# Performance work log

Measured on AMD Instinct MI355X. Metric: run time of the kernel, lower is better.

Reference implementation:

```python
import jax, jax.numpy as jnp
import numpy as np

A = 9
C = 80
TOPK = 1000            # topk_candidates
NMS_THRESH = 0.5
SCORE_THRESH = 0.05
DET_PER_IMG = 100      # detections_per_img
BBOX_XFORM_CLIP = float(np.log(1000.0 / 16.0))
CLASS_OFFSET = 4096.0  # > any clipped coordinate -> class-aware NMS trick


def setup_inputs() -> dict:
    key = jax.random.key(0)
    ks = jax.random.split(key, 4)
    B = 8
    levels = [(128, 128, 4096, 8), (64, 64, 2048, 16), (32, 32, 1024, 32)]  # H, W, K, stride
    inp = {}
    for i, (H, W, K, stride) in enumerate(levels):
        k1, k2, k3, k4, k5, k6, k7, k8 = jax.random.split(ks[i], 8)
        # plausible anchor boxes (x1, y1, x2, y2) with positive width/height
        cx = jax.random.uniform(k1, (B, H, W, A)) * (W * stride)
        cy = jax.random.uniform(k2, (B, H, W, A)) * (H * stride)
        w = 16.0 + jax.random.uniform(k3, (B, H, W, A)) * 112.0
        h = 16.0 + jax.random.uniform(k4, (B, H, W, A)) * 112.0
        anch = jnp.stack([cx - 0.5 * w, cy - 0.5 * h, cx + 0.5 * w, cy + 0.5 * h], axis=-1)
        # [B, H, W, A, 4] -> [B, 4A, H, W] (A groups of 4 along channel, matching permute(1,2,0) + reshape(-1,4))
        inp[f"anchors_{i}"] = jnp.transpose(anch.reshape(B, H, W, 4 * A), (0, 3, 1, 2)).astype(jnp.float32)
        coords = jnp.stack(
            [jax.random.randint(k5, (B, K), 0, H), jax.random.randint(k6, (B, K), 0, W)], axis=-1
        ).astype(jnp.int32)
        inp[f"coords_{i}"] = coords
        inp[f"score_logits_{i}"] = (jax.random.normal(k7, (B, K, A * C)) * 2.0 - 2.0).astype(jnp.float32)
        inp[f"regs_{i}"] = (jax.random.normal(k8, (B, K, A * 4)) * 0.2).astype(jnp.float32)
    inp["image_shapes"] = jnp.full((B, 2), 1024.0, dtype=jnp.float32)  # (h, w) per image
    return inp


def _decode(boxes, deltas, img_hw):
    # boxes, deltas: [N, 4] (x1, y1, x2, y2) / (dx, dy, dw, dh)
    x1, y1, x2, y2 = boxes[:, 0], boxes[:, 1], boxes[:, 2], boxes[:, 3]
    w = x2 - x1
    h = y2 - y1
    cx = x1 + 0.5 * w
    cy = y1 + 0.5 * h
    dx, dy = deltas[:, 0], deltas[:, 1]
    dw = jnp.minimum(deltas[:, 2], BBOX_XFORM_CLIP)
    dh = jnp.minimum(deltas[:, 3], BBOX_XFORM_CLIP)
    pcx = dx * w + cx
    pcy = dy * h + cy
    pw = jnp.exp(dw) * w
    ph = jnp.exp(dh) * h
    ih, iw = img_hw[0], img_hw[1]
    nx1 = jnp.clip(pcx - 0.5 * pw, 0.0, iw)
    ny1 = jnp.clip(pcy - 0.5 * ph, 0.0, ih)
    nx2 = jnp.clip(pcx + 0.5 * pw, 0.0, iw)
    ny2 = jnp.clip(pcy + 0.5 * ph, 0.0, ih)
    return jnp.stack([nx1, ny1, nx2, ny2], axis=-1)


def _level(anchor_map, coords, logits, regs, img_hw):
    # anchor_map: [4A, H, W]; coords: [K, 2]; logits: [K, A*C]; regs: [K, A*4]
    bb = jnp.transpose(anchor_map, (1, 2, 0))[coords[:, 0], coords[:, 1]]  # [K, 4A]
    boxes = bb.reshape(-1, 4)            # [K*A, 4]
    deltas = regs.reshape(-1, 4)         # [K*A, 4]
    dec = _decode(boxes, deltas, img_hw)
    scores = jax.nn.sigmoid(logits.reshape(-1, C))  # [K*A, C]
    flat = scores.reshape(-1)                       # [K*A*C]
    k = min(TOPK, flat.shape[0])
    top_s, idx = jax.lax.top_k(flat, k)
    return dec[idx // C], top_s, (idx % C)


def _pairwise_iou(b):
    area = (b[:, 2] - b[:, 0]) * (b[:, 3] - b[:, 1])
    lt = jnp.maximum(b[:, None, :2], b[None, :, :2])
    rb = jnp.minimum(b[:, None, 2:], b[None, :, 2:])
    wh = jnp.clip(rb - lt, 0.0)
    inter = wh[..., 0] * wh[..., 1]
    return inter / (area[:, None] + area[None, :] - inter + 1e-9)


def _nms(boxes, scores, labels):
    # class-aware NMS with fixed-size output [DET_PER_IMG, 6]
    order = jnp.argsort(-scores)
    b = boxes[order]
    s = scores[order]
    l = labels[order]
    iou = _pairwise_iou(b + l.astype(b.dtype)[:, None] * CLASS_OFFSET)  # [N, N]
    N = s.shape[0]
    idxs = jnp.arange(N)
    valid = s > SCORE_THRESH

    def body(i, keep):
        sup = (iou[i] > NMS_THRESH) & (idxs > i) & keep[i]
        return keep & ~sup

    keep = jax.lax.fori_loop(0, N, body, valid)
    masked = jnp.where(keep, s, -1.0)
    top_s, top_i = jax.lax.top_k(masked, DET_PER_IMG)
    pad = top_s > 0.0
    out_b = jnp.where(pad[:, None], b[top_i], 0.0)
    out_l = jnp.where(pad, l[top_i], -1).astype(b.dtype)
    return jnp.concatenate([out_b, top_s[:, None], out_l[:, None]], axis=-1)  # [DET, 6]


def _per_image(a0, a1, a2, c0, c1, c2, s0, s1, s2, r0, r1, r2, hw):
    parts = [
        _level(a, c, sl, r, hw)
        for a, c, sl, r in zip((a0, a1, a2), (c0, c1, c2), (s0, s1, s2), (r0, r1, r2))
    ]
    boxes = jnp.concatenate([p[0] for p in parts], axis=0)
    scores = jnp.concatenate([p[1] for p in parts], axis=0)
    labels = jnp.concatenate([p[2] for p in parts], axis=0)
    return _nms(boxes, scores, labels)


def reference(anchors_0, anchors_1, anchors_2, coords_0, coords_1, coords_2,
              score_logits_0, score_logits_1, score_logits_2,
              regs_0, regs_1, regs_2, image_shapes):
    # returns [B, DET_PER_IMG, 6] = (x1, y1, x2, y2, score, label); padded rows have score -1, label -1
    return jax.vmap(_per_image)(
        anchors_0, anchors_1, anchors_2,
        coords_0, coords_1, coords_2,
        score_logits_0, score_logits_1, score_logits_2,
        regs_0, regs_1, regs_2, image_shapes,
    )
```

## Files before the change

kernel.cpp:

```cpp
#include <hip/hip_runtime.h>

typedef unsigned long long u64;
typedef unsigned int u32;

#define NIMG 8
#define NLVL 3
#define TOPKN 1000
#define NC3 3000
#define DETS 100
#define PRETH 3.0f
#define NBINS 3072
#define LCAP 2048
#define MROWS 256
#define MLDS 128
#define NW 47
#define NWP 48
#define NSUB 32
#define SUBCAP 1536
#define GPAD 16

#define NBLK0 5760
#define NBLK1 2880
#define NBLK2 1440
#define NBLKTOT 10080

__device__ __forceinline__ u32 fmap(float f) {
  u32 b = __float_as_uint(f);
  return (b & 0x80000000u) ? ~b : (b | 0x80000000u);
}
__device__ __forceinline__ float funmap(u32 u) {
  u32 b = (u & 0x80000000u) ? (u & 0x7FFFFFFFu) : ~u;
  return __uint_as_float(b);
}

__global__ __launch_bounds__(256) void k_prefilter(
    const float* __restrict__ lg0, const float* __restrict__ lg1,
    const float* __restrict__ lg2, u64* __restrict__ dense,
    u32* __restrict__ gcnt) {
  const int tid = threadIdx.x, wave = tid >> 6, lane = tid & 63;
  int blk = blockIdx.x;
  const float* lg; int imgElems, lblk, lvl;
  if (blk < NBLK0)              { lg = lg0; imgElems = 2949120; lblk = blk; lvl = 0; }
  else if (blk < NBLK0 + NBLK1) { lg = lg1; imgElems = 1474560; lblk = blk - NBLK0; lvl = 1; }
  else                          { lg = lg2; imgElems = 737280;  lblk = blk - NBLK0 - NBLK1; lvl = 2; }
  int ce = lblk * 4096 + wave * 1024;
  int img = ce / imgElems;
  int flatBase = ce - img * imgElems;
  const float* src = lg + (size_t)img * imgElems;
  const int dst = img * NLVL + lvl;
  const int sub = (lblk * 4 + wave) & (NSUB - 1);
  u64 lmask = (1ull << lane) - 1ull;
  float va[16];
#pragma unroll
  for (int r = 0; r < 4; ++r) {
    const float4 v = *(const float4*)(src + flatBase + r * 256 + lane * 4);
    va[r * 4 + 0] = v.x; va[r * 4 + 1] = v.y;
    va[r * 4 + 2] = v.z; va[r * 4 + 3] = v.w;
  }
  u64 bm[16];
  int total = 0;
#pragma unroll
  for (int u = 0; u < 16; ++u) {
    bm[u] = __ballot(va[u] > PRETH);
    total += __popcll(bm[u]);
  }
  u32 base = 0;
  if (lane == 0 && total)
    base = atomicAdd(&gcnt[(dst * NSUB + sub) * GPAD], (u32)total);
  base = (u32)__shfl((int)base, 0);
  u64* db = dense + ((size_t)dst * NSUB + sub) * SUBCAP;
  int off = 0;
#pragma unroll
  for (int u = 0; u < 16; ++u) {
    u64 m = bm[u];
    if ((m >> lane) & 1ull) {
      int idx = flatBase + (u >> 2) * 256 + lane * 4 + (u & 3);
      u32 pos = base + (u32)(off + __popcll(m & lmask));
      if (pos < SUBCAP) db[pos] = ((u64)fmap(va[u]) << 32) | (u64)(~(u32)idx);
    }
    off += __popcll(m);
  }
}

__global__ __launch_bounds__(1024) void k_select(
    const u64* __restrict__ dense, const u32* __restrict__ gcnt,
    u64* __restrict__ topk) {
  __shared__ u32 hist[NBINS];
  __shared__ u64 lk[LCAP];
  __shared__ u32 wsum[16], wpre[16];
  __shared__ u32 scnt[NSUB];
  __shared__ int sT, sM;
  const int bi = blockIdx.x;
  const int tid = threadIdx.x, wave = tid >> 6, lane = tid & 63;

  const u64 SAFE = ((u64)0x3E5FFFFFu << 32) | 0xFFFFFFFFull;
  if (tid < TOPKN) topk[(size_t)bi * TOPKN + tid] = SAFE;
  for (int i = tid; i < NBINS; i += 1024) hist[i] = 0;
  if (tid < NSUB) {
    u32 c = gcnt[(bi * NSUB + tid) * GPAD];
    scnt[tid] = c > SUBCAP ? SUBCAP : c;
  }
  if (tid == 0) { sM = 0; sT = 0; }
  __syncthreads();

  const u64* src = dense + (size_t)bi * NSUB * SUBCAP;
  for (int s = wave; s < NSUB; s += 16) {
    u32 c = scnt[s];
    const u64* sp = src + (size_t)s * SUBCAP;
    for (u32 i = lane; i < c; i += 64) {
      u32 bin = ((u32)(sp[i] >> 32) - 0xC0000000u) >> 13;
      if (bin > NBINS - 1) bin = NBINS - 1;
      atomicAdd(&hist[bin], 1u);
    }
  }
  __syncthreads();

  const int h0 = NBINS - 1 - tid * 3;
  u32 a0 = hist[h0], a1 = hist[h0 - 1], a2 = hist[h0 - 2];
  u32 s = a0 + a1 + a2;
  u32 inc = s;
#pragma unroll
  for (int d = 1; d < 64; d <<= 1) {
    u32 t = (u32)__shfl_up((int)inc, d);
    if (lane >= d) inc += t;
  }
  if (lane == 63) wsum[wave] = inc;
  __syncthreads();
  if (tid < 16) {
    u32 w = wsum[tid];
    u32 wi = w;
#pragma unroll
    for (int d = 1; d < 16; d <<= 1) {
      u32 t = (u32)__shfl_up((int)wi, d);
      if (tid >= d) wi += t;
    }
    wpre[tid] = wi - w;
  }
  __syncthreads();
  u32 excl = wpre[wave] + (inc - s);
  if (excl < TOPKN && excl + s >= TOPKN) {
    u32 acc = excl + a0;
    int T;
    if (acc >= TOPKN) T = h0;
    else { acc += a1; T = (acc >= TOPKN) ? h0 - 1 : h0 - 2; }
    sT = T;
  }
  __syncthreads();
  const int T = sT;

  for (int s2 = wave; s2 < NSUB; s2 += 16) {
    u32 c = scnt[s2];
    const u64* sp = src + (size_t)s2 * SUBCAP;
    for (u32 i = lane; i < c; i += 64) {
      u64 key = sp[i];
      u32 bin = ((u32)(key >> 32) - 0xC0000000u) >> 13;
      if (bin > NBINS - 1) bin = NBINS - 1;
      if ((int)bin >= T) {
        int q = atomicAdd(&sM, 1);
        if (q < LCAP) lk[q] = key;
      }
    }
  }
  __syncthreads();
  int M = sM; if (M > LCAP) M = LCAP;
  u64 k0 = 0, k1 = 0;
  const bool have0 = tid < M, have1 = tid + 1024 < M;
  if (have0) k0 = lk[tid];
  if (have1) k1 = lk[tid + 1024];
  int r0 = 0, r1 = 0;
  for (int j = 0; j < M; ++j) {
    u64 kj = lk[j];
    r0 += (kj > k0);
    r1 += (kj > k1);
  }
  if (have0 && r0 < TOPKN) topk[(size_t)bi * TOPKN + r0] = k0;
  if (have1 && r1 < TOPKN) topk[(size_t)bi * TOPKN + r1] = k1;
}

__global__ __launch_bounds__(1024) void k_build(
    const u64* __restrict__ topk,
    const float* __restrict__ an0, const float* __restrict__ an1, const float* __restrict__ an2,
    const int* __restrict__ co0, const int* __restrict__ co1, const int* __restrict__ co2,
    const float* __restrict__ rg0, const float* __restrict__ rg1, const float* __restrict__ rg2,
    const float* __restrict__ ishape,
    float4* __restrict__ sbox, float* __restrict__ sscore, int* __restrict__ slabel) {
  __shared__ u64 keys[NC3];
  const int b = blockIdx.x, tid = threadIdx.x;
  const double ih = (double)ishape[b * 2 + 0];
  const double iw = (double)ishape[b * 2 + 1];
  const double CLIPV = 4.1351665567423563;
  float4 mb[3]; float ms[3]; int ml[3]; u64 mk[3]; bool mv[3];
  for (int q = 0; q < 3; ++q) {
    int c = tid + q * 1024;
    mv[q] = (c < NC3);
    mk[q] = 0ull;
    if (!mv[q]) continue;
    int l = c / 1000, pos = c - l * 1000;
    u64 key = topk[(size_t)(b * NLVL + l) * TOPKN + pos];
    u32 hi = (u32)(key >> 32);
    u32 flat = ~((u32)key);
    float logit = funmap(hi);
    int cls = (int)(flat % 80u);
    int bidx = (int)(flat / 80u);
    int k = bidx / 9, a = bidx - k * 9;
    const float* an; const int* co; const float* rg; int K, H, W;
    if (l == 0)      { an = an0; co = co0; rg = rg0; K = 4096; H = 128; W = 128; }
    else if (l == 1) { an = an1; co = co1; rg = rg1; K = 2048; H = 64;  W = 64;  }
    else             { an = an2; co = co2; rg = rg2; K = 1024; H = 32;  W = 32;  }
    if (k >= K) k = K - 1;
    int y = co[(b * K + k) * 2 + 0], x = co[(b * K + k) * 2 + 1];
    int HW = H * W;
    const float* ap = an + (size_t)(b * 36 + a * 4) * HW + y * W + x;
    double x1 = (double)ap[0], y1 = (double)ap[HW];
    double x2 = (double)ap[2 * HW], y2 = (double)ap[3 * HW];
    const float* rp = rg + (size_t)(b * K + k) * 36 + a * 4;
    double dx = (double)rp[0], dy = (double)rp[1];
    double dw = fmin((double)rp[2], CLIPV), dh = fmin((double)rp[3], CLIPV);
    double w = x2 - x1, h = y2 - y1;
    double cx = x1 + 0.5 * w, cy = y1 + 0.5 * h;
    double pcx = dx * w + cx, pcy = dy * h + cy;
    double pw = exp(dw) * w, ph = exp(dh) * h;
    double nx1 = fmin(fmax(pcx - 0.5 * pw, 0.0), iw);
    double ny1 = fmin(fmax(pcy - 0.5 * ph, 0.0), ih);
    double nx2 = fmin(fmax(pcx + 0.5 * pw, 0.0), iw);
    double ny2 = fmin(fmax(pcy + 0.5 * ph, 0.0), ih);
    mb[q] = make_float4((float)nx1, (float)ny1, (float)nx2, (float)ny2);
    ms[q] = (float)(1.0 / (1.0 + exp(-(double)logit)));
    ml[q] = cls;
    mk[q] = ((u64)hi << 32) | (u64)(~(u32)c);
    keys[c] = mk[q];
  }
  __syncthreads();
  for (int q = 0; q < 3; ++q) {
    if (!mv[q]) continue;
    int c = tid + q * 1024;
    int l = c / 1000, pos = c - l * 1000;
    int rank = pos;
    u64 key = mk[q];
#pragma unroll
    for (int m = 0; m < 3; ++m) {
      if (m == l) continue;
      int lo = 0, hi2 = 1000, base = m * 1000;
      while (lo < hi2) {
        int mid = (lo + hi2) >> 1;
        if (keys[base + mid] > key) lo = mid + 1; else hi2 = mid;
      }
      rank += lo;
    }
    sbox[(size_t)b * NC3 + rank] = mb[q];
    sscore[(size_t)b * NC3 + rank] = ms[q];
    slabel[(size_t)b * NC3 + rank] = ml[q];
  }
}

__global__ __launch_bounds__(256) void k_mask(
    const float4* __restrict__ sbox, const int* __restrict__ slabel,
    u64* __restrict__ mask) {
  __shared__ float4 qb[NC3];
  __shared__ float ar[NC3];
  const int img = blockIdx.x >> 4;
  const int r0 = (blockIdx.x & 15) * 16;
  const int tid = threadIdx.x, wave = tid >> 6, lane = tid & 63;
  for (int i = tid; i < NC3; i += 256) {
    float4 bx = sbox[(size_t)img * NC3 + i];
    float off = (float)slabel[(size_t)img * NC3 + i] * 4096.0f;
    float4 q = make_float4(bx.x + off, bx.y + off, bx.z + off, bx.w + off);
    qb[i] = q;
    ar[i] = (q.z - q.x) * (q.w - q.y);
  }
  __syncthreads();
  u64* mbase = mask + (size_t)img * MROWS * NWP;
  for (int q = 0; q < 4; ++q) {
    int i = r0 + wave * 4 + q;
    float4 bi = qb[i];
    float ai = ar[i];
    for (int w = 0; w < NW; ++w) {
      int j = w * 64 + lane;
      bool pred = false;
      if (j > i && j < NC3) {
        float4 bj = qb[j];
        float ltx = fmaxf(bi.x, bj.x), lty = fmaxf(bi.y, bj.y);
        float rbx = fminf(bi.z, bj.z), rby = fminf(bi.w, bj.w);
        float wx = fmaxf(rbx - ltx, 0.f), wy = fmaxf(rby - lty, 0.f);
        float inter = wx * wy;
        float denom = ((ai + ar[j]) - inter) + 1e-9f;
        pred = (inter / denom) > 0.5f;
      }
      u64 m = __ballot(pred);
      if (lane == 0) mbase[(size_t)i * NWP + w] = m;
    }
  }
}

__global__ __launch_bounds__(256) void k_serial(
    const float4* __restrict__ sbox, const float* __restrict__ sscore,
    const int* __restrict__ slabel, const u64* __restrict__ mask,
    float* __restrict__ out) {
  __shared__ u64 sm_mask[MLDS * NWP];
  __shared__ float sm_sc[NC3];
  __shared__ int keptIdx[DETS];
  __shared__ int s_cnt;
  const int img = blockIdx.x, tid = threadIdx.x, wave = tid >> 6, lane = tid & 63;
  const u64* mbase = mask + (size_t)img * MROWS * NWP;
  const float* sc = sscore + (size_t)img * NC3;
  for (int i = tid; i < MLDS * NWP; i += 256) sm_mask[i] = mbase[i];
  for (int i = tid; i < NC3; i += 256) sm_sc[i] = sc[i];
  __syncthreads();
  if (wave == 0) {
    u64 mykeep = 0;
    for (int w = 0; w < NW; ++w) {
      int j = w * 64 + lane;
      float s = (j < NC3) ? sm_sc[j] : -1.f;
      u64 m = __ballot(s > 0.05f);
      if (lane == w) mykeep = m;
    }
    u64 pend[4];
    for (int d = 0; d < 4; ++d)
      pend[d] = (lane < NW) ? sm_mask[d * NWP + lane] : 0ull;
    int cnt = 0;
    for (int i = 0; i < NC3; ++i) {
      u64 row = pend[i & 3];
      int nxt = i + 4;
      if (nxt < MROWS)
        pend[i & 3] = (lane < NW)
            ? ((nxt < MLDS) ? sm_mask[nxt * NWP + lane]
                            : mbase[(size_t)nxt * NWP + lane])
            : 0ull;
      int w = i >> 6;
      u64 kw = __shfl(mykeep, w);
      if ((kw >> (i & 63)) & 1ull) {
        if (lane == 0) keptIdx[cnt] = i;
        cnt++;
        if (cnt == DETS) break;
        if (i < MROWS) {
          mykeep &= ~row;
        } else {
          float4 bx = sbox[(size_t)img * NC3 + i];
          float off = (float)slabel[(size_t)img * NC3 + i] * 4096.0f;
          float bix = bx.x + off, biy = bx.y + off;
          float biz = bx.z + off, biw = bx.w + off;
          float ai = (biz - bix) * (biw - biy);
          for (int w2 = 0; w2 < NW; ++w2) {
            int j = w2 * 64 + lane;
            bool pred = false;
            if (j > i && j < NC3) {
              float4 bj = sbox[(size_t)img * NC3 + j];
              float o2 = (float)slabel[(size_t)img * NC3 + j] * 4096.0f;
              float jx = bj.x + o2, jy = bj.y + o2;
              float jz = bj.z + o2, jw = bj.w + o2;
              float aj = (jz - jx) * (jw - jy);
              float ltx = fmaxf(bix, jx), lty = fmaxf(biy, jy);
              float rbx = fminf(biz, jz), rby = fminf(biw, jw);
              float wx = fmaxf(rbx - ltx, 0.f), wy = fmaxf(rby - lty, 0.f);
              float inter = wx * wy;
              float denom = ((ai + aj) - inter) + 1e-9f;
              pred = (inter / denom) > 0.5f;
            }
            u64 m = __ballot(pred);
            if (lane == w2) mykeep &= ~m;
          }
        }
      }
    }
    if (lane == 0) s_cnt = cnt;
  }
  __syncthreads();
  const int cnt = s_cnt;
  for (int s = tid; s < DETS; s += 256) {
    float* o = out + ((size_t)img * DETS + s) * 6;
    if (s < cnt) {
      int i = keptIdx[s];
      float4 bx = sbox[(size_t)img * NC3 + i];
      o[0] = bx.x; o[1] = bx.y; o[2] = bx.z; o[3] = bx.w;
      o[4] = sm_sc[i];
      o[5] = (float)slabel[(size_t)img * NC3 + i];
    } else {
      o[0] = 0.f; o[1] = 0.f; o[2] = 0.f; o[3] = 0.f;
      o[4] = -1.0f; o[5] = -1.0f;
    }
  }
}

extern "C" void kernel_launch(void* const* d_in, const int* in_sizes, int n_in,
                              void* d_out, int out_size, void* d_ws, size_t ws_size,
                              hipStream_t stream) {
  int ia0, ic0, is0, ir0, ia1, ic1, is1, ir1, ia2, ic2, is2, ir2, ihw;
  if (in_sizes[1] == 8 * 4096 * 2) {
    ia0 = 0; ic0 = 1; is0 = 2; ir0 = 3;
    ia1 = 4; ic1 = 5; is1 = 6; ir1 = 7;
    ia2 = 8; ic2 = 9; is2 = 10; ir2 = 11; ihw = 12;
  } else {
    ia0 = 0; ia1 = 1; ia2 = 2;
    ic0 = 3; ic1 = 4; ic2 = 5;
    is0 = 6; is1 = 7; is2 = 8;
    ir0 = 9; ir1 = 10; ir2 = 11; ihw = 12;
  }

  u32* gcnt = (u32*)d_ws;
  u64* dense = (u64*)((char*)d_ws + 49152);
  u64* topk = dense + (size_t)NIMG * NLVL * NSUB * SUBCAP;
  float4* sboxp = (float4*)(topk + NIMG * NLVL * TOPKN);
  float* sscore = (float*)(sboxp + NIMG * NC3);
  int* slabel = (int*)(sscore + NIMG * NC3);
  u64* maskp = (u64*)(slabel + NIMG * NC3);
  float* out = (float*)d_out;

  hipMemsetAsync(d_ws, 0, 49152, stream);

  k_prefilter<<<NBLKTOT, 256, 0, stream>>>(
      (const float*)d_in[is0], (const float*)d_in[is1], (const float*)d_in[is2],
      dense, gcnt);
  k_select<<<NIMG * NLVL, 1024, 0, stream>>>(dense, gcnt, topk);
  k_build<<<NIMG, 1024, 0, stream>>>(topk,
      (const float*)d_in[ia0], (const float*)d_in[ia1], (const float*)d_in[ia2],
      (const int*)d_in[ic0], (const int*)d_in[ic1], (const int*)d_in[ic2],
      (const float*)d_in[ir0], (const float*)d_in[ir1], (const float*)d_in[ir2],
      (const float*)d_in[ihw],
      sboxp, sscore, slabel);
  k_mask<<<NIMG * 16, 256, 0, stream>>>(sboxp, slabel, maskp);
  k_serial<<<NIMG, 256, 0, stream>>>(sboxp, sscore, slabel, maskp, out);
}
```

Baseline: 390.9 us.

## Split box decode across more blocks, fuse mask and serial NMS kernels

The decode/rank kernel now runs 8 blocks per image, each decoding 375 candidates after every block rebuilds the full shared key array. The IoU mask kernel and the serial NMS kernel are merged into one 1024-thread block per image that reuses dynamic shared memory, removing one launch. Prefilter atomics are spread over 64 sub-buckets instead of 32, and a scheduling barrier is added after the loads. In exchange, mask computation for each image now runs on a single block instead of 16, and every decode block redoes the full key load.

```diff
diff --git a/kernel.cpp b/kernel.cpp
--- a/kernel.cpp
+++ b/kernel.cpp
@@ -15,9 +15,10 @@
 #define MLDS 128
 #define NW 47
 #define NWP 48
-#define NSUB 32
-#define SUBCAP 1536
+#define NSUB 64
+#define SUBCAP 768
 #define GPAD 16
+#define BG 8
 
 #define NBLK0 5760
 #define NBLK1 2880
@@ -57,6 +58,7 @@
     va[r * 4 + 0] = v.x; va[r * 4 + 1] = v.y;
     va[r * 4 + 2] = v.z; va[r * 4 + 3] = v.w;
   }
+  __builtin_amdgcn_sched_barrier(0);
   u64 bm[16];
   int total = 0;
 #pragma unroll
@@ -177,7 +179,7 @@
   if (have1 && r1 < TOPKN) topk[(size_t)bi * TOPKN + r1] = k1;
 }
 
-__global__ __launch_bounds__(1024) void k_build(
+__global__ __launch_bounds__(512) void k_build(
     const u64* __restrict__ topk,
     const float* __restrict__ an0, const float* __restrict__ an1, const float* __restrict__ an2,
     const int* __restrict__ co0, const int* __restrict__ co1, const int* __restrict__ co2,
@@ -185,16 +187,19 @@
     const float* __restrict__ ishape,
     float4* __restrict__ sbox, float* __restrict__ sscore, int* __restrict__ slabel) {
   __shared__ u64 keys[NC3];
-  const int b = blockIdx.x, tid = threadIdx.x;
+  const int bb = blockIdx.x, b = bb >> 3, g = bb & (BG - 1);
+  const int tid = threadIdx.x;
   const double ih = (double)ishape[b * 2 + 0];
   const double iw = (double)ishape[b * 2 + 1];
   const double CLIPV = 4.1351665567423563;
-  float4 mb[3]; float ms[3]; int ml[3]; u64 mk[3]; bool mv[3];
-  for (int q = 0; q < 3; ++q) {
-    int c = tid + q * 1024;
-    mv[q] = (c < NC3);
-    mk[q] = 0ull;
-    if (!mv[q]) continue;
+  for (int c = tid; c < NC3; c += 512) {
+    int l = c / 1000, pos = c - l * 1000;
+    u64 key = topk[(size_t)(b * NLVL + l) * TOPKN + pos];
+    keys[c] = (key & 0xFFFFFFFF00000000ull) | (u64)(~(u32)c);
+  }
+  __syncthreads();
+  if (tid < 375) {
+    int c = g * 375 + tid;
     int l = c / 1000, pos = c - l * 1000;
     u64 key = topk[(size_t)(b * NLVL + l) * TOPKN + pos];
     u32 hi = (u32)(key >> 32);
@@ -224,44 +229,38 @@
     double ny1 = fmin(fmax(pcy - 0.5 * ph, 0.0), ih);
     double nx2 = fmin(fmax(pcx + 0.5 * pw, 0.0), iw);
     double ny2 = fmin(fmax(pcy + 0.5 * ph, 0.0), ih);
-    mb[q] = make_float4((float)nx1, (float)ny1, (float)nx2, (float)ny2);
-    ms[q] = (float)(1.0 / (1.0 + exp(-(double)logit)));
-    ml[q] = cls;
-    mk[q] = ((u64)hi << 32) | (u64)(~(u32)c);
-    keys[c] = mk[q];
-  }
-  __syncthreads();
-  for (int q = 0; q < 3; ++q) {
-    if (!mv[q]) continue;
-    int c = tid + q * 1024;
-    int l = c / 1000, pos = c - l * 1000;
+    float4 mb = make_float4((float)nx1, (float)ny1, (float)nx2, (float)ny2);
+    float ms = (float)(1.0 / (1.0 + exp(-(double)logit)));
+    u64 mykey = keys[c];
     int rank = pos;
-    u64 key = mk[q];
 #pragma unroll
     for (int m = 0; m < 3; ++m) {
       if (m == l) continue;
       int lo = 0, hi2 = 1000, base = m * 1000;
       while (lo < hi2) {
         int mid = (lo + hi2) >> 1;
-        if (keys[base + mid] > key) lo = mid + 1; else hi2 = mid;
+        if (keys[base + mid] > mykey) lo = mid + 1; else hi2 = mid;
       }
       rank += lo;
     }
-    sbox[(size_t)b * NC3 + rank] = mb[q];
-    sscore[(size_t)b * NC3 + rank] = ms[q];
-    slabel[(size_t)b * NC3 + rank] = ml[q];
-  }
-}
-
-__global__ __launch_bounds__(256) void k_mask(
-    const float4* __restrict__ sbox, const int* __restrict__ slabel,
-    u64* __restrict__ mask) {
-  __shared__ float4 qb[NC3];
-  __shared__ float ar[NC3];
-  const int img = blockIdx.x >> 4;
-  const int r0 = (blockIdx.x & 15) * 16;
-  const int tid = threadIdx.x, wave = tid >> 6, lane = tid & 63;
-  for (int i = tid; i < NC3; i += 256) {
+    sbox[(size_t)b * NC3 + rank] = mb;
+    sscore[(size_t)b * NC3 + rank] = ms;
+    slabel[(size_t)b * NC3 + rank] = cls;
+  }
+}
+
+__global__ __launch_bounds__(1024) void k_nms(
+    const float4* __restrict__ sbox, const float* __restrict__ sscore,
+    const int* __restrict__ slabel, u64* __restrict__ mask,
+    float* __restrict__ out) {
+  extern __shared__ char smem[];
+  __shared__ int keptIdx[DETS];
+  __shared__ int s_cnt;
+  const int img = blockIdx.x, tid = threadIdx.x, wave = tid >> 6, lane = tid & 63;
+
+  float4* qb = (float4*)smem;
+  float* ar = (float*)(smem + 48000);
+  for (int i = tid; i < NC3; i += 1024) {
     float4 bx = sbox[(size_t)img * NC3 + i];
     float off = (float)slabel[(size_t)img * NC3 + i] * 4096.0f;
     float4 q = make_float4(bx.x + off, bx.y + off, bx.z + off, bx.w + off);
@@ -270,8 +269,8 @@
   }
   __syncthreads();
   u64* mbase = mask + (size_t)img * MROWS * NWP;
-  for (int q = 0; q < 4; ++q) {
-    int i = r0 + wave * 4 + q;
+  for (int q = 0; q < 16; ++q) {
+    int i = wave * 16 + q;
     float4 bi = qb[i];
     float ai = ar[i];
     for (int w = 0; w < NW; ++w) {
@@ -290,40 +289,32 @@
       if (lane == 0) mbase[(size_t)i * NWP + w] = m;
     }
   }
-}
-
-__global__ __launch_bounds__(256) void k_serial(
-    const float4* __restrict__ sbox, const float* __restrict__ sscore,
-    const int* __restrict__ slabel, const u64* __restrict__ mask,
-    float* __restrict__ out) {
-  __shared__ u64 sm_mask[MLDS * NWP];
-  __shared__ float sm_sc[NC3];
-  __shared__ int keptIdx[DETS];
-  __shared__ int s_cnt;
-  const int img = blockIdx.x, tid = threadIdx.x, wave = tid >> 6, lane = tid & 63;
-  const u64* mbase = mask + (size_t)img * MROWS * NWP;
-  const float* sc = sscore + (size_t)img * NC3;
-  for (int i = tid; i < MLDS * NWP; i += 256) sm_mask[i] = mbase[i];
-  for (int i = tid; i < NC3; i += 256) sm_sc[i] = sc[i];
+  __syncthreads();
+
+  u64* smask = (u64*)smem;
+  float* sc = (float*)(smem + 49152);
+  const float* scg = sscore + (size_t)img * NC3;
+  for (int i = tid; i < MLDS * NWP; i += 1024) smask[i] = mbase[i];
+  for (int i = tid; i < NC3; i += 1024) sc[i] = scg[i];
   __syncthreads();
   if (wave == 0) {
     u64 mykeep = 0;
     for (int w = 0; w < NW; ++w) {
       int j = w * 64 + lane;
-      float s = (j < NC3) ? sm_sc[j] : -1.f;
+      float s = (j < NC3) ? sc[j] : -1.f;
       u64 m = __ballot(s > 0.05f);
       if (lane == w) mykeep = m;
     }
     u64 pend[4];
     for (int d = 0; d < 4; ++d)
-      pend[d] = (lane < NW) ? sm_mask[d * NWP + lane] : 0ull;
+      pend[d] = (lane < NW) ? smask[d * NWP + lane] : 0ull;
     int cnt = 0;
     for (int i = 0; i < NC3; ++i) {
       u64 row = pend[i & 3];
       int nxt = i + 4;
       if (nxt < MROWS)
         pend[i & 3] = (lane < NW)
-            ? ((nxt < MLDS) ? sm_mask[nxt * NWP + lane]
+            ? ((nxt < MLDS) ? smask[nxt * NWP + lane]
                             : mbase[(size_t)nxt * NWP + lane])
             : 0ull;
       int w = i >> 6;
@@ -366,13 +357,13 @@
   }
   __syncthreads();
   const int cnt = s_cnt;
-  for (int s = tid; s < DETS; s += 256) {
+  for (int s = tid; s < DETS; s += 1024) {
     float* o = out + ((size_t)img * DETS + s) * 6;
     if (s < cnt) {
       int i = keptIdx[s];
       float4 bx = sbox[(size_t)img * NC3 + i];
       o[0] = bx.x; o[1] = bx.y; o[2] = bx.z; o[3] = bx.w;
-      o[4] = sm_sc[i];
+      o[4] = sc[i];
       o[5] = (float)slabel[(size_t)img * NC3 + i];
     } else {
       o[0] = 0.f; o[1] = 0.f; o[2] = 0.f; o[3] = 0.f;
@@ -397,7 +388,7 @@
   }
 
   u32* gcnt = (u32*)d_ws;
-  u64* dense = (u64*)((char*)d_ws + 49152);
+  u64* dense = (u64*)((char*)d_ws + 98304);
   u64* topk = dense + (size_t)NIMG * NLVL * NSUB * SUBCAP;
   float4* sboxp = (float4*)(topk + NIMG * NLVL * TOPKN);
   float* sscore = (float*)(sboxp + NIMG * NC3);
@@ -405,18 +396,17 @@
   u64* maskp = (u64*)(slabel + NIMG * NC3);
   float* out = (float*)d_out;
 
-  hipMemsetAsync(d_ws, 0, 49152, stream);
+  hipMemsetAsync(d_ws, 0, 98304, stream);
 
   k_prefilter<<<NBLKTOT, 256, 0, stream>>>(
       (const float*)d_in[is0], (const float*)d_in[is1], (const float*)d_in[is2],
       dense, gcnt);
   k_select<<<NIMG * NLVL, 1024, 0, stream>>>(dense, gcnt, topk);
-  k_build<<<NIMG, 1024, 0, stream>>>(topk,
+  k_build<<<NIMG * BG, 512, 0, stream>>>(topk,
       (const float*)d_in[ia0], (const float*)d_in[ia1], (const float*)d_in[ia2],
       (const int*)d_in[ic0], (const int*)d_in[ic1], (const int*)d_in[ic2],
       (const float*)d_in[ir0], (const float*)d_in[ir1], (const float*)d_in[ir2],
       (const float*)d_in[ihw],
       sboxp, sscore, slabel);
-  k_mask<<<NIMG * 16, 256, 0, stream>>>(sboxp, slabel, maskp);
-  k_serial<<<NIMG, 256, 0, stream>>>(sboxp, sscore, slabel, maskp, out);
-}
+  k_nms<<<NIMG, 1024, 61440, stream>>>(sboxp, sscore, slabel, maskp, out);
+}
```

New measurement: 641.5 us. 64.1% more time.
